# Kernel tuning notes

Measured on AMD Instinct MI355X. Metric: run time of the kernel, lower is better.

## Reference

```python
import jax, jax.numpy as jnp
import numpy as np

N_EXPERTS, D_IN, D_OUT = 8, 1024, 1024
N_TOKENS = 8192


def setup_inputs() -> dict:
    key = jax.random.key(0)
    ks = jax.random.split(key, 5)
    s_in = 1.0 / np.sqrt(D_IN)
    x = jax.random.normal(ks[0], (N_TOKENS, D_IN), dtype=jnp.float32)
    W = jax.random.uniform(ks[1], (N_EXPERTS, D_IN, D_OUT), jnp.float32, -s_in, s_in)
    b = jax.random.uniform(ks[2], (N_EXPERTS, D_OUT), jnp.float32, -s_in, s_in)
    gate_W = jax.random.uniform(ks[3], (D_IN, N_EXPERTS), jnp.float32, -s_in, s_in)
    gate_b = jax.random.uniform(ks[4], (N_EXPERTS,), jnp.float32, -s_in, s_in)
    return {"x": x, "W": W, "b": b, "gate_W": gate_W, "gate_b": gate_b}


def reference(x, W, b, gate_W, gate_b):
    # gate: [n, e] softmax over experts
    gate_score = jax.nn.softmax(x @ gate_W + gate_b, axis=-1)
    # all experts applied densely: [n, e, o]
    expert_outputs = jnp.einsum('ni,eio->neo', x, W) + b[None, :, :]
    # weighted combine over expert axis: [n, o]
    return jnp.einsum('ne,neo->no', gate_score, expert_outputs)
```

## Files before the change

kernel.cpp:

```cpp
#include <hip/hip_runtime.h>
#include <hip/hip_bf16.h>
#include <cstdint>
#include <cstddef>

#define N_TOK 8192
#define D_IN  1024
#define D_OUT 1024
#define N_EXP 8
#define KTOT  (N_EXP * D_IN)

#define BM    256
#define BN    128
#define BKH   32
#define NSTEP 256

typedef __attribute__((ext_vector_type(8))) short short8;
typedef __attribute__((ext_vector_type(8))) unsigned short ushort8;
typedef __attribute__((ext_vector_type(4))) float f32x4;

__device__ __forceinline__ unsigned short f2bf(float f) {
    union { float f; unsigned int u; } v; v.f = f;
    return (unsigned short)((v.u + 0x7FFFu + ((v.u >> 16) & 1u)) >> 16);
}

__device__ __forceinline__ void load_lds16(const void* g, void* l) {
    __builtin_amdgcn_global_load_lds(
        (const __attribute__((address_space(1))) void*)g,
        (__attribute__((address_space(3))) void*)l,
        16, 0, 0);
}

__global__ __launch_bounds__(256) void prep_kernel(
    const float* __restrict__ x, const float* __restrict__ gW,
    const float* __restrict__ gbias, const float* __restrict__ W,
    unsigned short* __restrict__ xb, unsigned short* __restrict__ Wt,
    float* __restrict__ g_t) {
    const int b = blockIdx.x;
    const int t = threadIdx.x;

    __shared__ __align__(16) float smem[8 * 1028];

    if (b < 2048) {
        float (*tile)[65] = (float(*)[65])smem;
        const int e  = b >> 8;
        const int i0 = ((b >> 4) & 15) * 64;
        const int o0 = (b & 15) * 64;

        const int rr = t >> 4;
        const int rc = (t & 15) * 4;
#pragma unroll
        for (int j = 0; j < 4; ++j) {
            const float4 v = *(const float4*)(
                W + ((size_t)e * D_IN + (i0 + rr + 16 * j)) * D_OUT + o0 + rc);
            tile[rr + 16 * j][rc + 0] = v.x;
            tile[rr + 16 * j][rc + 1] = v.y;
            tile[rr + 16 * j][rc + 2] = v.z;
            tile[rr + 16 * j][rc + 3] = v.w;
        }
        __syncthreads();
        const int ow = t >> 2;
        const int c  = (t & 3) * 16;
        ushort8 v0, v1;
#pragma unroll
        for (int j = 0; j < 8; ++j) v0[j] = f2bf(tile[c + j][ow]);
#pragma unroll
        for (int j = 0; j < 8; ++j) v1[j] = f2bf(tile[c + 8 + j][ow]);
        unsigned short* dst = Wt + (size_t)(o0 + ow) * KTOT + e * D_IN + i0 + c;
        *(ushort8*)dst = v0;
        *(ushort8*)(dst + 8) = v1;
    } else {
        float (*gwT)[1028] = (float(*)[1028])smem;
#pragma unroll
        for (int r = 0; r < 32; ++r) {
            const int flat = t + 256 * r;
            gwT[flat & 7][flat >> 3] = gW[flat];
        }
        __syncthreads();

        const int lane = t & 63;
        const int n    = (b - 2048) * 4 + (t >> 6);

        float acc[8];
#pragma unroll
        for (int e = 0; e < 8; ++e) acc[e] = 0.f;
#pragma unroll
        for (int jj = 0; jj < 4; ++jj) {
            const int i = 256 * jj + 4 * lane;
            const float4 xv = *(const float4*)(x + (size_t)n * D_IN + i);
            ushort4 u;
            u.x = f2bf(xv.x); u.y = f2bf(xv.y);
            u.z = f2bf(xv.z); u.w = f2bf(xv.w);
            *(ushort4*)(xb + (size_t)n * D_IN + i) = u;
#pragma unroll
            for (int e = 0; e < 8; ++e) {
                const float4 wv = *(const float4*)&gwT[e][i];
                acc[e] += xv.x * wv.x + xv.y * wv.y
                        + xv.z * wv.z + xv.w * wv.w;
            }
        }
#pragma unroll
        for (int off = 32; off > 0; off >>= 1) {
#pragma unroll
            for (int e = 0; e < 8; ++e) acc[e] += __shfl_down(acc[e], off);
        }
        if (lane == 0) {
            float lg[8], mx = -1e30f;
#pragma unroll
            for (int e = 0; e < 8; ++e) {
                lg[e] = acc[e] + gbias[e];
                mx = fmaxf(mx, lg[e]);
            }
            float s = 0.f;
#pragma unroll
            for (int e = 0; e < 8; ++e) { lg[e] = expf(lg[e] - mx); s += lg[e]; }
            const float inv = 1.f / s;
#pragma unroll
            for (int e = 0; e < 8; ++e)
                g_t[(size_t)e * N_TOK + n] = lg[e] * inv;
        }
    }
}

__global__ __launch_bounds__(512, 1) void moe_gemm13_kernel(
    const unsigned short* __restrict__ xb,
    const unsigned short* __restrict__ Wt,
    const float* __restrict__ bias,
    const float* __restrict__ g_t,
    float* __restrict__ out) {
    __shared__ __align__(16) unsigned short A4[4][BM * BKH];
    __shared__ __align__(16) unsigned short B4[4][BN * BKH];
    __shared__ __align__(16) float g_s[N_EXP][BM];
    __shared__ __align__(16) float r_s[N_EXP][BM];
    __shared__ __align__(16) float b_s[N_EXP][BN];

    const int t    = threadIdx.x;
    const int lane = t & 63;
    const int ln15 = lane & 15;
    const int quad = lane >> 4;
    const int wave = t >> 6;
    const int wm0  = (wave >> 1) * 64;
    const int wn0  = (wave & 1) * 64;

    const int flat = blockIdx.x + 8 * blockIdx.y;
    const int bn0  = ((flat >> 3) & 7) * BN;
    const int bm0  = ((flat & 7) * 4 + (flat >> 6)) * BM;

    for (int j = t; j < N_EXP * BM; j += 512)
        g_s[j >> 8][j & 255] = g_t[(size_t)(j >> 8) * N_TOK + bm0 + (j & 255)];
    for (int j = t; j < N_EXP * BN; j += 512)
        b_s[j >> 7][j & 127] = bias[(size_t)(j >> 7) * D_OUT + bn0 + (j & 127)];
    __syncthreads();
    if (t < BM) {
        float d[N_EXP];
#pragma unroll
        for (int e = 0; e < N_EXP; ++e) d[e] = fmaxf(g_s[e][t], 1e-30f);
#pragma unroll
        for (int e = 1; e < N_EXP; ++e) r_s[e][t] = d[e - 1] / d[e];
        r_s[0][t] = d[N_EXP - 1];
    }
    __syncthreads();

    f32x4 acc[4][4];
#pragma unroll
    for (int mi = 0; mi < 4; ++mi)
#pragma unroll
        for (int ni = 0; ni < 4; ++ni)
            acc[mi][ni] = (f32x4){0.f, 0.f, 0.f, 0.f};

    const int srow = t >> 2;
    const int csw  = ((t & 3) ^ ((t >> 3) & 3)) * 8;
    const unsigned short* gA = xb + (size_t)(bm0 + srow) * D_IN + csw;
    const unsigned short* gB = Wt + (size_t)(bn0 + srow) * (size_t)KTOT + csw;
    const int wrow = wave * 16 * BKH;

    const int ksw  = (quad ^ ((ln15 >> 1) & 3)) * 8;
    const int aoff = (wm0 + ln15) * BKH + ksw;
    const int boff = (wn0 + ln15) * BKH + ksw;

    short8 afA[4], bvA[4], afB[4], bvB[4];

#pragma unroll
    for (int s = 0; s < 3; ++s) {
        load_lds16(gA + s * BKH,              &A4[s][wrow]);
        load_lds16(gA + 128 * D_IN + s * BKH, &A4[s][128 * BKH + wrow]);
        load_lds16(gB + (size_t)s * BKH,      &B4[s][wrow]);
    }
    asm volatile("s_waitcnt vmcnt(3)" ::: "memory");
    __builtin_amdgcn_s_barrier();
    __builtin_amdgcn_sched_barrier(0);
#pragma unroll
    for (int mi = 0; mi < 4; ++mi)
        afA[mi] = *(const short8*)(&A4[0][0] + aoff + mi * 16 * BKH);
#pragma unroll
    for (int ni = 0; ni < 4; ++ni)
        bvA[ni] = *(const short8*)(&B4[0][0] + boff + ni * 16 * BKH);

#define MFMA4(CUR, mi_)                                                       \
    _Pragma("unroll") for (int ni = 0; ni < 4; ++ni)                          \
        acc[mi_][ni] = __builtin_amdgcn_mfma_f32_16x16x32_bf16(               \
            af##CUR[mi_], bv##CUR[ni], acc[mi_][ni], 0, 0, 0);

#define STEP(h_, CUR, NXT, DO_STAGE, DO_READ)                                 \
  {                                                                           \
    const int hs_ = (h_) + 3;                                                 \
    const unsigned short* An_ = &A4[((h_) + 1) & 3][0];                       \
    const unsigned short* Bn_ = &B4[((h_) + 1) & 3][0];                       \
    asm volatile("s_waitcnt lgkmcnt(0)" ::: "memory");                        \
    __builtin_amdgcn_sched_barrier(0);                                        \
    if ((h_) && !((h_) & 31)) {      \
      const int e_ = (h_) >> 5;                                               \
      _Pragma("unroll") for (int mi = 0; mi < 4; ++mi) {                      \
        const f32x4 rv = *(const f32x4*)&r_s[e_][wm0 + mi * 16 + quad * 4];   \
        _Pragma("unroll") for (int ni = 0; ni < 4; ++ni)                      \
          _Pragma("unroll") for (int r = 0; r < 4; ++r)                       \
            acc[mi][ni][r] *= rv[r];                                          \
      }                                                                       \
    }                                                                         \
    __builtin_amdgcn_s_setprio(1);                                            \
    MFMA4(CUR, 0)                                                             \
    __builtin_amdgcn_sched_barrier(0);                                        \
    if (DO_READ) {                                                            \
      af##NXT[0] = *(const short8*)(An_ + aoff + 0 * 16 * BKH);               \
      af##NXT[1] = *(const short8*)(An_ + aoff + 1 * 16 * BKH);               \
    }                                                                         \
    __builtin_amdgcn_sched_barrier(0);                                        \
    MFMA4(CUR, 1)                                                             \
    __builtin_amdgcn_sched_barrier(0);                                        \
    if (DO_READ) {                                                            \
      af##NXT[2] = *(const short8*)(An_ + aoff + 2 * 16 * BKH);               \
      af##NXT[3] = *(const short8*)(An_ + aoff + 3 * 16 * BKH);               \
    }                                                                         \
    __builtin_amdgcn_sched_barrier(0);                                        \
    MFMA4(CUR, 2)                                                             \
    __builtin_amdgcn_sched_barrier(0);                                        \
    if (DO_READ) {                                                            \
      _Pragma("unroll") for (int ni = 0; ni < 4; ++ni)                        \
        bv##NXT[ni] = *(const short8*)(Bn_ + boff + ni * 16 * BKH);           \
    }                                                                         \
    __builtin_amdgcn_sched_barrier(0);                                        \
    MFMA4(CUR, 3)                                                             \
    __builtin_amdgcn_s_setprio(0);                                            \
    __builtin_amdgcn_sched_barrier(0);                                        \
    if (DO_STAGE) {                                                           \
      load_lds16(gA + ((hs_) & 31) * BKH,              &A4[(hs_) & 3][wrow]); \
      load_lds16(gA + 128 * D_IN + ((hs_) & 31) * BKH,                        \
                 &A4[(hs_) & 3][128 * BKH + wrow]);                           \
      load_lds16(gB + (size_t)(hs_) * BKH,             &B4[(hs_) & 3][wrow]); \
    }                                                                         \
  }

#define ENDW(N_)                                                              \
  asm volatile("s_waitcnt vmcnt(" #N_ ")" ::: "memory");                      \
  __builtin_amdgcn_s_barrier();                                               \
  __builtin_amdgcn_sched_barrier(0);

    for (int h = 0; h < NSTEP - 4; h += 2) {
        STEP(h, A, B, 1, 1);
        ENDW(3);
        STEP(h + 1, B, A, 1, 1);
        ENDW(3);
    }
    STEP(252, A, B, 1, 1);
    ENDW(3);
    STEP(253, B, A, 0, 1);
    ENDW(0);
    STEP(254, A, B, 0, 1);
    STEP(255, B, A, 0, 0);

#undef STEP
#undef MFMA4
#undef ENDW

#pragma unroll
    for (int mi = 0; mi < 4; ++mi) {
        const f32x4 fin = *(const f32x4*)&r_s[0][wm0 + mi * 16 + quad * 4];
#pragma unroll
        for (int ni = 0; ni < 4; ++ni)
#pragma unroll
            for (int r = 0; r < 4; ++r) acc[mi][ni][r] *= fin[r];
    }
#pragma unroll
    for (int e = 0; e < N_EXP; ++e) {
        f32x4 gv[4];
        float bb[4];
#pragma unroll
        for (int mi = 0; mi < 4; ++mi)
            gv[mi] = *(const f32x4*)&g_s[e][wm0 + mi * 16 + quad * 4];
#pragma unroll
        for (int ni = 0; ni < 4; ++ni) bb[ni] = b_s[e][wn0 + ni * 16 + ln15];
#pragma unroll
        for (int mi = 0; mi < 4; ++mi)
#pragma unroll
            for (int ni = 0; ni < 4; ++ni)
#pragma unroll
                for (int r = 0; r < 4; ++r)
                    acc[mi][ni][r] += gv[mi][r] * bb[ni];
    }

#pragma unroll
    for (int mi = 0; mi < 4; ++mi) {
#pragma unroll
        for (int ni = 0; ni < 4; ++ni) {
            const int col  = bn0 + wn0 + ni * 16 + ln15;
            const int row0 = bm0 + wm0 + mi * 16 + quad * 4;
#pragma unroll
            for (int r = 0; r < 4; ++r)
                out[(size_t)(row0 + r) * D_OUT + col] = acc[mi][ni][r];
        }
    }
}

extern "C" void kernel_launch(void* const* d_in, const int* in_sizes, int n_in,
                              void* d_out, int out_size, void* d_ws, size_t ws_size,
                              hipStream_t stream) {
    const float* x  = (const float*)d_in[0];
    const float* W  = (const float*)d_in[1];
    const float* b  = (const float*)d_in[2];
    const float* gW = (const float*)d_in[3];
    const float* gb = (const float*)d_in[4];
    float* out = (float*)d_out;

    unsigned short* xb  = (unsigned short*)d_ws;
    unsigned short* Wt  = xb + (size_t)N_TOK * D_IN;
    float*          g_t = (float*)(Wt + (size_t)D_OUT * KTOT);

    prep_kernel<<<4096, 256, 0, stream>>>(x, gW, gb, W, xb, Wt, g_t);
    moe_gemm13_kernel<<<dim3(D_OUT / BN, N_TOK / BM), 512, 0, stream>>>(
        xb, Wt, b, g_t, out);
}
```

Baseline: 248.3 us.

## Halve block threads to 4 waves each computing 128x64 output tiles

Cuts the GEMM block from 8 waves to 4. Each wave now holds a 128x64 accumulator (8x4 MFMA tiles), which raises arithmetic intensity per LDS fragment read. Global-to-LDS staging is moved to the start of each step so the loads are issued before the MFMAs, and B fragment reads are interleaved with A reads. This roughly doubles accumulator register pressure and halves the waves available to hide latency.

```diff
diff --git a/kernel.cpp b/kernel.cpp
--- a/kernel.cpp
+++ b/kernel.cpp
@@ -121,7 +121,7 @@
     }
 }
 
-__global__ __launch_bounds__(512, 1) void moe_gemm13_kernel(
+__global__ __launch_bounds__(256, 1) void moe_gemm17_kernel(
     const unsigned short* __restrict__ xb,
     const unsigned short* __restrict__ Wt,
     const float* __restrict__ bias,
@@ -138,19 +138,19 @@
     const int ln15 = lane & 15;
     const int quad = lane >> 4;
     const int wave = t >> 6;
-    const int wm0  = (wave >> 1) * 64;
+    const int wm0  = (wave >> 1) * 128;
     const int wn0  = (wave & 1) * 64;
 
     const int flat = blockIdx.x + 8 * blockIdx.y;
     const int bn0  = ((flat >> 3) & 7) * BN;
     const int bm0  = ((flat & 7) * 4 + (flat >> 6)) * BM;
 
-    for (int j = t; j < N_EXP * BM; j += 512)
+    for (int j = t; j < N_EXP * BM; j += 256)
         g_s[j >> 8][j & 255] = g_t[(size_t)(j >> 8) * N_TOK + bm0 + (j & 255)];
-    for (int j = t; j < N_EXP * BN; j += 512)
+    for (int j = t; j < N_EXP * BN; j += 256)
         b_s[j >> 7][j & 127] = bias[(size_t)(j >> 7) * D_OUT + bn0 + (j & 127)];
     __syncthreads();
-    if (t < BM) {
+    {
         float d[N_EXP];
 #pragma unroll
         for (int e = 0; e < N_EXP; ++e) d[e] = fmaxf(g_s[e][t], 1e-30f);
@@ -160,93 +160,102 @@
     }
     __syncthreads();
 
-    f32x4 acc[4][4];
-#pragma unroll
-    for (int mi = 0; mi < 4; ++mi)
+    f32x4 acc[8][4];
+#pragma unroll
+    for (int mi = 0; mi < 8; ++mi)
 #pragma unroll
         for (int ni = 0; ni < 4; ++ni)
             acc[mi][ni] = (f32x4){0.f, 0.f, 0.f, 0.f};
 
-    const int srow = t >> 2;
     const int csw  = ((t & 3) ^ ((t >> 3) & 3)) * 8;
-    const unsigned short* gA = xb + (size_t)(bm0 + srow) * D_IN + csw;
-    const unsigned short* gB = Wt + (size_t)(bn0 + srow) * (size_t)KTOT + csw;
-    const int wrow = wave * 16 * BKH;
+    const unsigned short* gA = xb + (size_t)(bm0 + (t >> 2)) * D_IN + csw;
+    const unsigned short* gB = Wt + (size_t)(bn0 + (t >> 2)) * (size_t)KTOT + csw;
+    const int wb = wave * 16 * BKH;
 
     const int ksw  = (quad ^ ((ln15 >> 1) & 3)) * 8;
     const int aoff = (wm0 + ln15) * BKH + ksw;
     const int boff = (wn0 + ln15) * BKH + ksw;
 
-    short8 afA[4], bvA[4], afB[4], bvB[4];
-
-#pragma unroll
-    for (int s = 0; s < 3; ++s) {
-        load_lds16(gA + s * BKH,              &A4[s][wrow]);
-        load_lds16(gA + 128 * D_IN + s * BKH, &A4[s][128 * BKH + wrow]);
-        load_lds16(gB + (size_t)s * BKH,      &B4[s][wrow]);
-    }
-    asm volatile("s_waitcnt vmcnt(3)" ::: "memory");
+    short8 afA[8], afB[8], bvA[4], bvB[4];
+
+#define STAGE(h_, slot_)                                                      \
+  {                                                                           \
+    load_lds16(gA + ((h_) & 31) * BKH,               &A4[slot_][wb]);         \
+    load_lds16(gA + 64 * D_IN + ((h_) & 31) * BKH,   &A4[slot_][2048 + wb]);  \
+    load_lds16(gA + 128 * D_IN + ((h_) & 31) * BKH,  &A4[slot_][4096 + wb]);  \
+    load_lds16(gA + 192 * D_IN + ((h_) & 31) * BKH,  &A4[slot_][6144 + wb]);  \
+    load_lds16(gB + (size_t)(h_) * BKH,              &B4[slot_][wb]);         \
+    load_lds16(gB + 64 * (size_t)KTOT + (size_t)(h_) * BKH,                   \
+               &B4[slot_][2048 + wb]);                                        \
+  }
+
+    STAGE(0, 0) STAGE(1, 1) STAGE(2, 2)
+    asm volatile("s_waitcnt vmcnt(6)" ::: "memory");
     __builtin_amdgcn_s_barrier();
     __builtin_amdgcn_sched_barrier(0);
 #pragma unroll
-    for (int mi = 0; mi < 4; ++mi)
+    for (int mi = 0; mi < 8; ++mi)
         afA[mi] = *(const short8*)(&A4[0][0] + aoff + mi * 16 * BKH);
 #pragma unroll
     for (int ni = 0; ni < 4; ++ni)
         bvA[ni] = *(const short8*)(&B4[0][0] + boff + ni * 16 * BKH);
 
-#define MFMA4(CUR, mi_)                                                       \
-    _Pragma("unroll") for (int ni = 0; ni < 4; ++ni)                          \
-        acc[mi_][ni] = __builtin_amdgcn_mfma_f32_16x16x32_bf16(               \
-            af##CUR[mi_], bv##CUR[ni], acc[mi_][ni], 0, 0, 0);
+#define MFMA8(CUR, ni_)                                                       \
+    _Pragma("unroll") for (int mi = 0; mi < 8; ++mi)                          \
+        acc[mi][ni_] = __builtin_amdgcn_mfma_f32_16x16x32_bf16(               \
+            af##CUR[mi], bv##CUR[ni_], acc[mi][ni_], 0, 0, 0);
 
 #define STEP(h_, CUR, NXT, DO_STAGE, DO_READ)                                 \
   {                                                                           \
-    const int hs_ = (h_) + 3;                                                 \
     const unsigned short* An_ = &A4[((h_) + 1) & 3][0];                       \
     const unsigned short* Bn_ = &B4[((h_) + 1) & 3][0];                       \
     asm volatile("s_waitcnt lgkmcnt(0)" ::: "memory");                        \
     __builtin_amdgcn_sched_barrier(0);                                        \
     if ((h_) && !((h_) & 31)) {      \
       const int e_ = (h_) >> 5;                                               \
-      _Pragma("unroll") for (int mi = 0; mi < 4; ++mi) {                      \
+      _Pragma("unroll") for (int mi = 0; mi < 8; ++mi) {                      \
         const f32x4 rv = *(const f32x4*)&r_s[e_][wm0 + mi * 16 + quad * 4];   \
         _Pragma("unroll") for (int ni = 0; ni < 4; ++ni)                      \
           _Pragma("unroll") for (int r = 0; r < 4; ++r)                       \
             acc[mi][ni][r] *= rv[r];                                          \
       }                                                                       \
     }                                                                         \
+    if (DO_STAGE) STAGE((h_) + 3, ((h_) + 3) & 3)                             \
+    __builtin_amdgcn_sched_barrier(0);                                        \
     __builtin_amdgcn_s_setprio(1);                                            \
-    MFMA4(CUR, 0)                                                             \
+    MFMA8(CUR, 0)                                                             \
     __builtin_amdgcn_sched_barrier(0);                                        \
     if (DO_READ) {                                                            \
+      bv##NXT[0] = *(const short8*)(Bn_ + boff + 0 * 16 * BKH);               \
       af##NXT[0] = *(const short8*)(An_ + aoff + 0 * 16 * BKH);               \
       af##NXT[1] = *(const short8*)(An_ + aoff + 1 * 16 * BKH);               \
     }                                                                         \
     __builtin_amdgcn_sched_barrier(0);                                        \
-    MFMA4(CUR, 1)                                                             \
+    MFMA8(CUR, 1)                                                             \
     __builtin_amdgcn_sched_barrier(0);                                        \
     if (DO_READ) {                                                            \
+      bv##NXT[1] = *(const short8*)(Bn_ + boff + 1 * 16 * BKH);               \
       af##NXT[2] = *(const short8*)(An_ + aoff + 2 * 16 * BKH);               \
       af##NXT[3] = *(const short8*)(An_ + aoff + 3 * 16 * BKH);               \
     }                                                                         \
     __builtin_amdgcn_sched_barrier(0);                                        \
-    MFMA4(CUR, 2)                                                             \
+    MFMA8(CUR, 2)                                                             \
     __builtin_amdgcn_sched_barrier(0);                                        \
     if (DO_READ) {                                                            \
-      _Pragma("unroll") for (int ni = 0; ni < 4; ++ni)                        \
-        bv##NXT[ni] = *(const short8*)(Bn_ + boff + ni * 16 * BKH);           \
-    }                                                                         \
-    __builtin_amdgcn_sched_barrier(0);                                        \
-    MFMA4(CUR, 3)                                                             \
+      bv##NXT[2] = *(const short8*)(Bn_ + boff + 2 * 16 * BKH);               \
+      af##NXT[4] = *(const short8*)(An_ + aoff + 4 * 16 * BKH);               \
+      af##NXT[5] = *(const short8*)(An_ + aoff + 5 * 16 * BKH);               \
+    }                                                                         \
+    __builtin_amdgcn_sched_barrier(0);                                        \
+    MFMA8(CUR, 3)                                                             \
+    __builtin_amdgcn_sched_barrier(0);                                        \
+    if (DO_READ) {                                                            \
+      bv##NXT[3] = *(const short8*)(Bn_ + boff + 3 * 16 * BKH);               \
+      af##NXT[6] = *(const short8*)(An_ + aoff + 6 * 16 * BKH);               \
+      af##NXT[7] = *(const short8*)(An_ + aoff + 7 * 16 * BKH);               \
+    }                                                                         \
     __builtin_amdgcn_s_setprio(0);                                            \
     __builtin_amdgcn_sched_barrier(0);                                        \
-    if (DO_STAGE) {                                                           \
-      load_lds16(gA + ((hs_) & 31) * BKH,              &A4[(hs_) & 3][wrow]); \
-      load_lds16(gA + 128 * D_IN + ((hs_) & 31) * BKH,                        \
-                 &A4[(hs_) & 3][128 * BKH + wrow]);                           \
-      load_lds16(gB + (size_t)(hs_) * BKH,             &B4[(hs_) & 3][wrow]); \
-    }                                                                         \
   }
 
 #define ENDW(N_)                                                              \
@@ -256,23 +265,24 @@
 
     for (int h = 0; h < NSTEP - 4; h += 2) {
         STEP(h, A, B, 1, 1);
-        ENDW(3);
+        ENDW(6);
         STEP(h + 1, B, A, 1, 1);
-        ENDW(3);
+        ENDW(6);
     }
     STEP(252, A, B, 1, 1);
-    ENDW(3);
+    ENDW(6);
     STEP(253, B, A, 0, 1);
     ENDW(0);
     STEP(254, A, B, 0, 1);
     STEP(255, B, A, 0, 0);
 
 #undef STEP
-#undef MFMA4
+#undef MFMA8
 #undef ENDW
-
-#pragma unroll
-    for (int mi = 0; mi < 4; ++mi) {
+#undef STAGE
+
+#pragma unroll
+    for (int mi = 0; mi < 8; ++mi) {
         const f32x4 fin = *(const f32x4*)&r_s[0][wm0 + mi * 16 + quad * 4];
 #pragma unroll
         for (int ni = 0; ni < 4; ++ni)
@@ -281,15 +291,15 @@
     }
 #pragma unroll
     for (int e = 0; e < N_EXP; ++e) {
-        f32x4 gv[4];
+        f32x4 gv[8];
         float bb[4];
 #pragma unroll
-        for (int mi = 0; mi < 4; ++mi)
+        for (int mi = 0; mi < 8; ++mi)
             gv[mi] = *(const f32x4*)&g_s[e][wm0 + mi * 16 + quad * 4];
 #pragma unroll
         for (int ni = 0; ni < 4; ++ni) bb[ni] = b_s[e][wn0 + ni * 16 + ln15];
 #pragma unroll
-        for (int mi = 0; mi < 4; ++mi)
+        for (int mi = 0; mi < 8; ++mi)
 #pragma unroll
             for (int ni = 0; ni < 4; ++ni)
 #pragma unroll
@@ -298,7 +308,7 @@
     }
 
 #pragma unroll
-    for (int mi = 0; mi < 4; ++mi) {
+    for (int mi = 0; mi < 8; ++mi) {
 #pragma unroll
         for (int ni = 0; ni < 4; ++ni) {
             const int col  = bn0 + wn0 + ni * 16 + ln15;
@@ -325,6 +335,6 @@
     float*          g_t = (float*)(Wt + (size_t)D_OUT * KTOT);
 
     prep_kernel<<<4096, 256, 0, stream>>>(x, gW, gb, W, xb, Wt, g_t);
-    moe_gemm13_kernel<<<dim3(D_OUT / BN, N_TOK / BM), 512, 0, stream>>>(
+    moe_gemm17_kernel<<<dim3(D_OUT / BN, N_TOK / BM), 256, 0, stream>>>(
         xb, Wt, b, g_t, out);
 }
```

New measurement: 295.3 us. +18.9%, slower.
